# Performance work log

Hardware: AMD Instinct MI355X
Metric: run time of the kernel (lower is better)

The kernel has to match this reference:

```python
import jax, jax.numpy as jnp
import numpy as np
from jax import lax

REGION_SIZE = 5      # local window side (init kwarg)
BANDWIDTH = 0.1      # KDE kernel bandwidth (init kwarg)
NUM_BINS = 256       # intensity histogram bins
EPS = 1e-10


def setup_inputs() -> dict:
    key = jax.random.key(0)
    # image-like inputs in [0, 255] to match the 256 intensity bins
    x = jax.random.uniform(key, (8, 3, 96, 96), dtype=jnp.float32) * 255.0
    return {"x": x}


def reference(x):
    # x: [B, C, H, W]
    bins = jnp.arange(NUM_BINS, dtype=x.dtype)            # [256]
    # derivative-of-sigmoid KDE kernel evaluated at each (pixel, bin) pair
    d = (x[..., None] - bins) / BANDWIDTH                 # [B,C,H,W,256]
    sig = jax.nn.sigmoid(d)
    k = sig * (1.0 - sig)                                 # [B,C,H,W,256]
    # accumulate kernel mass over the region_size x region_size window
    # (stride 1, centered -> SAME padding), per bin
    p = lax.reduce_window(
        k, jnp.float32(0.0), lax.add,
        window_dimensions=(1, 1, REGION_SIZE, REGION_SIZE, 1),
        window_strides=(1, 1, 1, 1, 1),
        padding='SAME')                                   # [B,C,H,W,256]
    # normalize to a probability distribution over bins
    p = p / (jnp.sum(p, axis=-1, keepdims=True) + EPS)
    # Shannon entropy per pixel
    return -jnp.sum(p * jnp.log(p + EPS), axis=-1)        # [B,C,H,W]
```

## Files before the change

kernel.cpp:

```cpp
#include <hip/hip_runtime.h>
#include <hip/hip_fp16.h>
#include <stdint.h>


#define W   96
#define H   96
#define WP  100
#define IMG (W*H)
#define IMGP (WP*WP)
#define TPB 256

#if __has_builtin(__builtin_amdgcn_logf)
__device__ __forceinline__ float rawlog2(float v) {
    return __builtin_amdgcn_logf(v);
}
#else
__device__ __forceinline__ float rawlog2(float v) {
    float r;
    asm("v_log_f32 %0, %1\n\ts_nop 1" : "=v"(r) : "v"(v));
    return r;
}
#endif

__global__ __launch_bounds__(TPB) void mass_kernel(
    const float* __restrict__ x, uint2* __restrict__ wm, int total2)
{
    const int pid = blockIdx.x * TPB + threadIdx.x;
    if (pid >= total2) return;
    const int x2  = pid % WP;
    const int y2  = (pid / WP) % WP;
    const int img = pid / IMGP;

    uint2 e;
    if (x2 >= 2 && x2 < WP - 2 && y2 >= 2 && y2 < WP - 2) {
        const float v  = x[img * IMG + (y2 - 2) * W + (x2 - 2)];
        const int   b0 = (int)v;
        const float f  = v - (float)b0;
        const float E  = __expf(-10.f * f);
        const float E2 = __expf(10.f * f - 10.f);
        const float r0 = __builtin_amdgcn_rcpf(1.f + E);
        const float r1 = __builtin_amdgcn_rcpf(1.f + E2);
        const float k0 = E  * r0 * r0;
        const float k1 = E2 * r1 * r1;
        const __half2 hk = __floats2half2_rn(k0, k1);
        e.x = __builtin_bit_cast(uint32_t, hk);
        e.y = (uint32_t)(b0 << 4);
    } else {
        e.x = 0u;
        e.y = (uint32_t)(1 << 20);
    }
    wm[pid] = e;
}

__global__ __launch_bounds__(TPB) void entropy_kde_kernel(
    const uint2* __restrict__ wm, float* __restrict__ out)
{
    const int px   = blockIdx.x * TPB + threadIdx.x;
    const int xcol = px % W;
    const int y    = (px / W) % H;
    const int img  = px / IMG;
    const uint2* __restrict__ wb = wm + img * IMGP + y * WP + xcol;

    uint32_t pk [25];
    int      bsh[25];
    uint32_t P  [25];

    #pragma unroll
    for (int i = 0; i < 25; ++i) {
        const uint2 m = wb[(i / 5) * WP + (i % 5)];
        pk[i]  = m.x;
        bsh[i] = (int)m.y;
        P[i]   = 0u;
    }

    #pragma unroll
    for (int j = 0; j < 24; ++j) {
        const uint64_t pkj = ((uint64_t)pk[j]) << 32;
        const int      cj  = 32 - bsh[j];
        #pragma unroll
        for (int i = j + 1; i < 25; ++i) {
            int s = bsh[i] + cj;
            s = s < 0 ? 0 : (s > 63 ? 63 : s);
            const uint32_t t = (uint32_t)(pkj >> s);
            const __half2 sum = __hadd2(__builtin_bit_cast(__half2, P[i]),
                                        __builtin_bit_cast(__half2, t));
            P[i] = __builtin_bit_cast(uint32_t, sum);
        }
    }

    float S0 = 0.f, S1 = 0.f;
    float T0 = 0.f, T1 = 0.f, T2a = 0.f, T3 = 0.f;
    #pragma unroll
    for (int i = 0; i < 25; ++i) {
        const float2 kc = __half22float2(__builtin_bit_cast(__half2, pk[i]));
        const float2 Pv = __half22float2(__builtin_bit_cast(__half2, P[i]));
        if (i & 1) S1 += kc.x + kc.y; else S0 += kc.x + kc.y;
        const float z0 = Pv.x + kc.x, z1 = Pv.y + kc.y;
        const float t4 = z0 * rawlog2(z0 + 1e-10f) - Pv.x * rawlog2(Pv.x + 1e-10f)
                       + z1 * rawlog2(z1 + 1e-10f) - Pv.y * rawlog2(Pv.y + 1e-10f);
        if      ((i & 3) == 0) T0  += t4;
        else if ((i & 3) == 1) T1  += t4;
        else if ((i & 3) == 2) T2a += t4;
        else                   T3  += t4;
    }

    const float S = (S0 + S1) + 1e-10f;
    const float T = (T0 + T1) + (T2a + T3);
    out[px] = 0.69314718056f * (rawlog2(S) - T / S);
}

extern "C" void kernel_launch(void* const* d_in, const int* in_sizes, int n_in,
                              void* d_out, int out_size, void* d_ws, size_t ws_size,
                              hipStream_t stream)
{
    const float* x = (const float*)d_in[0];
    float* out = (float*)d_out;
    uint2* wm  = (uint2*)d_ws;
    const int total  = in_sizes[0];
    const int total2 = (total / IMG) * IMGP;
    mass_kernel<<<(total2 + TPB - 1) / TPB, TPB, 0, stream>>>(x, wm, total2);
    entropy_kde_kernel<<<total / TPB, TPB, 0, stream>>>(wm, out);
}
```

Before: 70.26 us.

## Split per-pixel pairwise entropy work across two wavefronts and combine via LDS

Each output pixel is now handled by two wavefronts. One computes the pairwise bin-overlap terms for window elements 0-16 and the other for 17-24, and the partial S and T sums are merged through shared memory before the final entropy. This doubles the thread count and lowers per-thread serial work and register pressure, so there is more parallelism across the GPU. In exchange it adds a __syncthreads and an LDS exchange, and the split is uneven: the 0-16 role does about 136 pair updates against about 164 for the 17-24 role.

After: 69.40 us. About the same (-1.2%).

```diff
diff --git a/kernel.cpp b/kernel.cpp
--- a/kernel.cpp
+++ b/kernel.cpp
@@ -52,61 +52,82 @@
     wm[pid] = e;
 }
 
+template<int I0, int I1>
+__device__ __forceinline__ void role_compute(const uint2* __restrict__ wb,
+                                             float& Sout, float& Tout)
+{
+    uint32_t pk[I1]; int bsh[I1];
+    #pragma unroll
+    for (int i = 0; i < I1; ++i) {
+        const uint2 m = wb[(i / 5) * WP + (i % 5)];
+        pk[i]  = m.x;
+        bsh[i] = (int)m.y;
+    }
+
+    uint32_t P[I1 - I0];
+    #pragma unroll
+    for (int t = 0; t < I1 - I0; ++t) P[t] = 0u;
+
+    #pragma unroll
+    for (int j = 0; j < I1 - 1; ++j) {
+        const uint64_t pkj = ((uint64_t)pk[j]) << 32;
+        const int      cj  = 32 - bsh[j];
+        #pragma unroll
+        for (int i = (j + 1 > I0 ? j + 1 : I0); i < I1; ++i) {
+            int s = bsh[i] + cj;
+            s = s < 0 ? 0 : (s > 63 ? 63 : s);
+            const uint32_t t = (uint32_t)(pkj >> s);
+            const __half2 sum = __hadd2(__builtin_bit_cast(__half2, P[i - I0]),
+                                        __builtin_bit_cast(__half2, t));
+            P[i - I0] = __builtin_bit_cast(uint32_t, sum);
+        }
+    }
+
+    float S0 = 0.f, S1 = 0.f;
+    float T0 = 0.f, T1 = 0.f;
+    #pragma unroll
+    for (int i = I0; i < I1; ++i) {
+        const float2 kc = __half22float2(__builtin_bit_cast(__half2, pk[i]));
+        const float2 Pv = __half22float2(__builtin_bit_cast(__half2, P[i - I0]));
+        if (i & 1) S1 += kc.x + kc.y; else S0 += kc.x + kc.y;
+        const float z0 = Pv.x + kc.x, z1 = Pv.y + kc.y;
+        const float t4 = z0 * rawlog2(z0 + 1e-10f) - Pv.x * rawlog2(Pv.x + 1e-10f)
+                       + z1 * rawlog2(z1 + 1e-10f) - Pv.y * rawlog2(Pv.y + 1e-10f);
+        if (i & 1) T1 += t4; else T0 += t4;
+    }
+    Sout = S0 + S1;
+    Tout = T0 + T1;
+}
+
 __global__ __launch_bounds__(TPB) void entropy_kde_kernel(
-    const uint2* __restrict__ wm, float* __restrict__ out)
+    const uint2* __restrict__ wm, float* __restrict__ out, int total)
 {
-    const int px   = blockIdx.x * TPB + threadIdx.x;
+    __shared__ float sS[128], sT[128];
+    const int tid  = threadIdx.x;
+    const int wv   = tid >> 6;
+    const int g    = wv >> 1;
+    const int r    = wv & 1;
+    const int wl   = tid & 63;
+    const int slot = g * 64 + wl;
+    const int px   = blockIdx.x * 128 + slot;
+
     const int xcol = px % W;
     const int y    = (px / W) % H;
     const int img  = px / IMG;
     const uint2* __restrict__ wb = wm + img * IMGP + y * WP + xcol;
 
-    uint32_t pk [25];
-    int      bsh[25];
-    uint32_t P  [25];
+    float S, T;
+    if (r == 0) role_compute<0, 17>(wb, S, T);
+    else        role_compute<17, 25>(wb, S, T);
 
-    #pragma unroll
-    for (int i = 0; i < 25; ++i) {
-        const uint2 m = wb[(i / 5) * WP + (i % 5)];
-        pk[i]  = m.x;
-        bsh[i] = (int)m.y;
-        P[i]   = 0u;
+    if (r == 1) { sS[slot] = S; sT[slot] = T; }
+    __syncthreads();
+    if (r == 0) {
+        S += sS[slot];
+        T += sT[slot];
+        const float Sp = S + 1e-10f;
+        if (px < total) out[px] = 0.69314718056f * (rawlog2(Sp) - T / Sp);
     }
-
-    #pragma unroll
-    for (int j = 0; j < 24; ++j) {
-        const uint64_t pkj = ((uint64_t)pk[j]) << 32;
-        const int      cj  = 32 - bsh[j];
-        #pragma unroll
-        for (int i = j + 1; i < 25; ++i) {
-            int s = bsh[i] + cj;
-            s = s < 0 ? 0 : (s > 63 ? 63 : s);
-            const uint32_t t = (uint32_t)(pkj >> s);
-            const __half2 sum = __hadd2(__builtin_bit_cast(__half2, P[i]),
-                                        __builtin_bit_cast(__half2, t));
-            P[i] = __builtin_bit_cast(uint32_t, sum);
-        }
-    }
-
-    float S0 = 0.f, S1 = 0.f;
-    float T0 = 0.f, T1 = 0.f, T2a = 0.f, T3 = 0.f;
-    #pragma unroll
-    for (int i = 0; i < 25; ++i) {
-        const float2 kc = __half22float2(__builtin_bit_cast(__half2, pk[i]));
-        const float2 Pv = __half22float2(__builtin_bit_cast(__half2, P[i]));
-        if (i & 1) S1 += kc.x + kc.y; else S0 += kc.x + kc.y;
-        const float z0 = Pv.x + kc.x, z1 = Pv.y + kc.y;
-        const float t4 = z0 * rawlog2(z0 + 1e-10f) - Pv.x * rawlog2(Pv.x + 1e-10f)
-                       + z1 * rawlog2(z1 + 1e-10f) - Pv.y * rawlog2(Pv.y + 1e-10f);
-        if      ((i & 3) == 0) T0  += t4;
-        else if ((i & 3) == 1) T1  += t4;
-        else if ((i & 3) == 2) T2a += t4;
-        else                   T3  += t4;
-    }
-
-    const float S = (S0 + S1) + 1e-10f;
-    const float T = (T0 + T1) + (T2a + T3);
-    out[px] = 0.69314718056f * (rawlog2(S) - T / S);
 }
 
 extern "C" void kernel_launch(void* const* d_in, const int* in_sizes, int n_in,
@@ -119,5 +140,5 @@
     const int total  = in_sizes[0];
     const int total2 = (total / IMG) * IMGP;
     mass_kernel<<<(total2 + TPB - 1) / TPB, TPB, 0, stream>>>(x, wm, total2);
-    entropy_kde_kernel<<<total / TPB, TPB, 0, stream>>>(wm, out);
+    entropy_kde_kernel<<<total / 128, TPB, 0, stream>>>(wm, out, total);
 }
```
